# Performance work log

Measured on AMD Instinct MI355X. Metric: run time of the kernel, lower is better.

The kernel has to match this reference:

```python
import jax, jax.numpy as jnp
import numpy as np

EPS = 1e-5  # torch LayerNorm default

def ln(x, g, b):
    mu = jnp.mean(x, axis=-1, keepdims=True)
    var = jnp.mean((x - mu) ** 2, axis=-1, keepdims=True)
    return (x - mu) * jax.lax.rsqrt(var + EPS) * g + b

B, S, E, A = 131072, 199, 3, 32
D_IN = S + 1  # state_dim + 1 (time feature)

def setup_inputs() -> dict:
    key = jax.random.key(0)
    ks = iter(jax.random.split(key, 32))
    def w(shape, fan_in):
        lim = 1.0 / np.sqrt(fan_in)
        return jax.random.uniform(next(ks), shape, jnp.float32, -lim, lim)
    inp = {
        "state": jax.random.normal(next(ks), (B, S), jnp.float32),
        "time_delta": jax.random.uniform(next(ks), (B,), jnp.float32),
        # trunk: Linear(200,256)+LN, Linear(256,256)+LN, Linear(256,128)+LN
        "W1": w((D_IN, 256), D_IN), "b1": w((256,), D_IN),
        "g1": jnp.ones((256,), jnp.float32), "be1": jnp.zeros((256,), jnp.float32),
        "W2": w((256, 256), 256), "b2": w((256,), 256),
        "g2": jnp.ones((256,), jnp.float32), "be2": jnp.zeros((256,), jnp.float32),
        "W3": w((256, 128), 256), "b3": w((128,), 256),
        "g3": jnp.ones((128,), jnp.float32), "be3": jnp.zeros((128,), jnp.float32),
        # value stream
        "Wv1": w((128, 64), 128), "bv1": w((64,), 128),
        "gv": jnp.ones((64,), jnp.float32), "bev": jnp.zeros((64,), jnp.float32),
        "Wv2": w((64, 1), 64), "bv2": w((1,), 64),
        # E stacked advantage streams (all heads share action dim A)
        "Wa1": w((E, 128, 64), 128), "ba1": w((E, 64), 128),
        "ga": jnp.ones((E, 64), jnp.float32), "bea": jnp.zeros((E, 64), jnp.float32),
        "Wa2": w((E, 64, A), 64), "ba2": w((E, A), 64),
        "event_type": jax.random.randint(next(ks), (B,), 0, E),
    }
    return inp

def reference(state, time_delta,
              W1, b1, g1, be1, W2, b2, g2, be2, W3, b3, g3, be3,
              Wv1, bv1, gv, bev, Wv2, bv2,
              Wa1, ba1, ga, bea, Wa2, ba2, event_type):
    td = time_delta[:, None]                       # [B,1]
    x = jnp.concatenate([state, td], axis=1)       # [B,200]
    h = jax.nn.relu(ln(x @ W1 + b1, g1, be1))      # [B,256]
    h = jax.nn.relu(ln(h @ W2 + b2, g2, be2))      # [B,256]
    f = jax.nn.relu(ln(h @ W3 + b3, g3, be3))      # [B,128]
    v = jax.nn.relu(ln(f @ Wv1 + bv1, gv, bev)) @ Wv2 + bv2  # [B,1]
    # compute all E advantage heads, then per-sample select by event_type
    h1 = jnp.einsum('bd,edh->ebh', f, Wa1) + ba1[:, None, :]           # [E,B,64]
    h1 = jax.nn.relu(ln(h1, ga[:, None, :], bea[:, None, :]))
    adv_all = jnp.einsum('ebh,eha->eba', h1, Wa2) + ba2[:, None, :]    # [E,B,A]
    adv = jnp.take_along_axis(adv_all, event_type[None, :, None], axis=0)[0]  # [B,A]
    return v + (adv - adv.mean(axis=1, keepdims=True))
```

## Files before the change

kernel.cpp:

```cpp
#include <hip/hip_runtime.h>
#include <stdint.h>

#define DEV __device__ __forceinline__

typedef __attribute__((ext_vector_type(8))) short short8;
typedef __attribute__((ext_vector_type(4))) short short4v;
typedef __attribute__((ext_vector_type(4))) float floatx4;

constexpr int TM  = 64;
constexpr int NB  = 131072;
constexpr int AST = 264;

constexpr int OFF_W1 = 0;
constexpr int OFF_W2 = 57344;
constexpr int OFF_W3 = 122880;
constexpr int OFF_WH = 155648;
constexpr int OFF_WA2= 188416;
constexpr int NWQ    = 194560;

constexpr int C_B1=0, C_G1=256, C_BE1=512, C_B2=768, C_G2=1024, C_BE2=1280,
  C_B3=1536, C_G3=1664, C_BE3=1792, C_BV1=1920, C_GV=1984, C_BEV=2048,
  C_WV2=2112, C_BV2=2176, C_BA1=2177, C_GA=2369, C_BEA=2561, C_BA2=2753;
constexpr int NCONST=2849;

struct Ptrs {
  const float *state,*td,*W1,*b1,*g1,*be1,*W2,*b2,*g2,*be2,*W3,*b3,*g3,*be3,
    *Wv1,*bv1,*gv,*bev,*Wv2,*bv2,*Wa1,*ba1,*ga,*bea,*Wa2,*ba2;
  const int *et;
};

DEV unsigned short f2bf(float x){
  uint32_t u = __float_as_uint(x);
  u += 0x7fffu + ((u>>16)&1u);
  return (unsigned short)(u>>16);
}

__global__ void prep_kernel(Ptrs p, unsigned short* __restrict__ wq, float* __restrict__ cq){
  int idx = blockIdx.x*256 + threadIdx.x;
  if (idx < NWQ) {
    float v = 0.f;
    if (idx < OFF_W2) {
      int e = idx, w = e/14336, r = e%14336;
      int kc = r>>11, ct=(r>>9)&3, l=(r>>3)&63, j=r&7;
      int n = w*64 + ct*16 + (l&15);
      int k = kc*32 + (l>>4)*8 + j;
      if (k < 200) v = p.W1[k*256 + n];
    } else if (idx < OFF_W3) {
      int e = idx-OFF_W2, w=e>>14, r=e&16383;
      int kc=r>>11, ct=(r>>9)&3, l=(r>>3)&63, j=r&7;
      int n = w*64 + ct*16 + (l&15);
      int k = kc*32 + (l>>4)*8 + j;
      int c = (k & ~63) + 16*(k&3) + ((k&63)>>2);
      v = p.W2[c*256 + n];
    } else if (idx < OFF_WH) {
      int e = idx-OFF_W3, w=e>>13, r=e&8191;
      int kc=r>>10, ct=(r>>9)&1, l=(r>>3)&63, j=r&7;
      int n = w*32 + ct*16 + (l&15);
      int k = kc*32 + (l>>4)*8 + j;
      int c = (k & ~63) + 16*(k&3) + ((k&63)>>2);
      v = p.W3[c*128 + n];
    } else if (idx < OFF_WA2) {
      int e = idx-OFF_WH, h=e>>13, r=e&8191;
      int kc=r>>11, ct=(r>>9)&3, l=(r>>3)&63, j=r&7;
      int n = ct*16 + (l&15);
      int k = kc*32 + (l>>4)*8 + j;
      int c = (k & ~31) + 16*(k&1) + ((k&31)>>1);
      v = (h<3) ? p.Wa1[h*8192 + c*64 + n] : p.Wv1[c*64 + n];
    } else {
      int e = idx-OFF_WA2, h=e>>11, r=e&2047;
      int kc=r>>10, ct=(r>>9)&1, l=(r>>3)&63, j=r&7;
      int n = ct*16 + (l&15);
      int k = kc*32 + (l>>4)*8 + j;
      int c = 16*(k&3) + (k>>2);
      v = p.Wa2[h*2048 + c*32 + n];
    }
    wq[idx] = f2bf(v);
  } else if (idx < NWQ + NCONST) {
    int ci = idx - NWQ;
    const float* src; int off;
    if      (ci < 256)  { src=p.b1;  off=ci; }
    else if (ci < 512)  { src=p.g1;  off=ci-256; }
    else if (ci < 768)  { src=p.be1; off=ci-512; }
    else if (ci < 1024) { src=p.b2;  off=ci-768; }
    else if (ci < 1280) { src=p.g2;  off=ci-1024; }
    else if (ci < 1536) { src=p.be2; off=ci-1280; }
    else if (ci < 1664) { src=p.b3;  off=ci-1536; }
    else if (ci < 1792) { src=p.g3;  off=ci-1664; }
    else if (ci < 1920) { src=p.be3; off=ci-1792; }
    else if (ci < 1984) { src=p.bv1; off=ci-1920; }
    else if (ci < 2048) { src=p.gv;  off=ci-1984; }
    else if (ci < 2112) { src=p.bev; off=ci-2048; }
    else if (ci < 2176) { src=p.Wv2; off=ci-2112; }
    else if (ci < 2177) { src=p.bv2; off=ci-2176; }
    else if (ci < 2369) { src=p.ba1; off=ci-2177; }
    else if (ci < 2561) { src=p.ga;  off=ci-2369; }
    else if (ci < 2753) { src=p.bea; off=ci-2561; }
    else                { src=p.ba2; off=ci-2753; }
    cq[ci] = src[off];
  }
}

template<int N>
DEV void loadB(short8 (&B)[N], const unsigned short* __restrict__ src, int lane){
  #pragma unroll
  for (int i=0;i<N;i++) B[i] = *(const short8*)(src + i*512 + lane*8);
}

template<int RT,int CT>
DEV void zeroAcc(floatx4 (&acc)[RT][CT]){
  const floatx4 z = {0.f,0.f,0.f,0.f};
  #pragma unroll
  for (int rt=0;rt<RT;rt++)
    #pragma unroll
    for (int ct=0;ct<CT;ct++) acc[rt][ct]=z;
}

template<int KC,int CT>
DEV void runGemm(floatx4 (&acc)[4][CT], const short8 (&B)[KC*CT],
                 const unsigned short* aBase, int aOff){
  #pragma unroll
  for (int kc=0;kc<KC;kc++){
    short8 a[4];
    #pragma unroll
    for (int rt=0;rt<4;rt++)
      a[rt] = *(const short8*)(aBase + rt*16*AST + aOff + kc*32);
    #pragma unroll
    for (int rt=0;rt<4;rt++)
      #pragma unroll
      for (int ct=0;ct<CT;ct++)
        acc[rt][ct] = __builtin_amdgcn_mfma_f32_16x16x32_bf16(a[rt], B[kc*CT+ct], acc[rt][ct], 0,0,0);
  }
}

template<int CT>
DEV void biasStatsWrite(floatx4 (&acc)[4][CT], const float* __restrict__ cq, int bo, int colBase,
                        float2* pstatw, int ln, int q){
  float bias[CT];
  #pragma unroll
  for (int ct=0;ct<CT;ct++) bias[ct]=cq[bo+colBase+ct*16+ln];
  #pragma unroll
  for (int rt=0;rt<4;rt++){
    float s[4]={0,0,0,0}, ss[4]={0,0,0,0};
    #pragma unroll
    for (int ct=0;ct<CT;ct++){
      #pragma unroll
      for (int r=0;r<4;r++){
        float v=acc[rt][ct][r]+bias[ct];
        acc[rt][ct][r]=v; s[r]+=v; ss[r]+=v*v;
      }
    }
    #pragma unroll
    for (int r=0;r<4;r++){
      #pragma unroll
      for (int d=1;d<16;d<<=1){ s[r]+=__shfl_xor(s[r],d); ss[r]+=__shfl_xor(ss[r],d); }
      if (ln==0) pstatw[rt*16+q*4+r] = make_float2(s[r], ss[r]);
    }
  }
}

template<int CT>
DEV void lnWrite(floatx4 (&acc)[4][CT], const float* __restrict__ cq, int go, int beo, int colBase,
                 const float2* fstat, unsigned short* act_, int ln, int q){
  float g[CT], be[CT];
  #pragma unroll
  for (int ct=0;ct<CT;ct++){ g[ct]=cq[go+colBase+ct*16+ln]; be[ct]=cq[beo+colBase+ct*16+ln]; }
  #pragma unroll
  for (int rt=0;rt<4;rt++){
    #pragma unroll
    for (int r=0;r<4;r++){
      int row=rt*16+q*4+r;
      float2 st=fstat[row];
      unsigned short* pp = act_ + row*AST + colBase + ln*CT;
      if constexpr (CT==4){
        short4v vv;
        #pragma unroll
        for (int ct=0;ct<CT;ct++){
          float y=(acc[rt][ct][r]-st.x)*st.y*g[ct]+be[ct];
          vv[ct]=(short)f2bf(fmaxf(y,0.f));
        }
        *(short4v*)pp = vv;
      } else {
        uint32_t pk=0;
        #pragma unroll
        for (int ct=0;ct<CT;ct++){
          float y=(acc[rt][ct][r]-st.x)*st.y*g[ct]+be[ct];
          pk |= ((uint32_t)f2bf(fmaxf(y,0.f)))<<(16*ct);
        }
        *(uint32_t*)pp = pk;
      }
    }
  }
}

__global__ __launch_bounds__(256,2) void dqn_main(
    const float* __restrict__ state, const float* __restrict__ td,
    const int* __restrict__ et, const unsigned short* __restrict__ wq,
    const float* __restrict__ cq, float* __restrict__ out)
{
  __shared__ __align__(16) unsigned short act[TM*AST];
  __shared__ float2 pstat[4*64];
  __shared__ float2 fstat[64];
  __shared__ float  advbuf[64*32];
  __shared__ float  vbuf[64];
  __shared__ int    etl[64];

  const int tid=threadIdx.x, w=tid>>6, lane=tid&63, q=lane>>4, ln=lane&15;
  const int rowBlk = blockIdx.x*TM;

  {
    int r = tid>>2, q4 = tid&3, c0 = q4*56;
    const float* srow = state + (size_t)(rowBlk+r)*199;
    float tdv = td[rowBlk+r];
    unsigned short* arow = act + r*AST;
    #pragma unroll
    for (int cc=0; cc<28; cc++){
      int c = c0 + cc*2;
      float v0 = (c  <199)? srow[c]   : (c  ==199? tdv : 0.f);
      float v1 = (c+1<199)? srow[c+1] : (c+1==199? tdv : 0.f);
      uint32_t pk = (uint32_t)f2bf(v0) | ((uint32_t)f2bf(v1)<<16);
      *(uint32_t*)(arow + c) = pk;
    }
    if (tid < 64) etl[tid] = et[rowBlk+tid];
  }
  __syncthreads();

  const unsigned short* aBase = act + ln*AST + q*8;
  floatx4 acc[4][4];

  {
    short8 B[28];
    loadB<28>(B, wq + OFF_W1 + w*14336, lane);
    zeroAcc<4,4>(acc);
    runGemm<7,4>(acc, B, aBase, 0);
  }
  biasStatsWrite<4>(acc, cq, C_B1, w*64, &pstat[w*64], ln, q);
  __syncthreads();
  if (tid<64){
    float s=0, ss=0;
    #pragma unroll
    for (int ww=0;ww<4;ww++){ float2 pp=pstat[ww*64+tid]; s+=pp.x; ss+=pp.y; }
    float mu=s*(1.f/256.f), var=ss*(1.f/256.f)-mu*mu;
    fstat[tid]=make_float2(mu, rsqrtf(var+1e-5f));
  }
  __syncthreads();
  lnWrite<4>(acc, cq, C_G1, C_BE1, w*64, fstat, act, ln, q);
  __syncthreads();

  {
    short8 B[32];
    loadB<32>(B, wq + OFF_W2 + w*16384, lane);
    zeroAcc<4,4>(acc);
    runGemm<8,4>(acc, B, aBase, 0);
  }
  biasStatsWrite<4>(acc, cq, C_B2, w*64, &pstat[w*64], ln, q);
  __syncthreads();
  if (tid<64){
    float s=0, ss=0;
    #pragma unroll
    for (int ww=0;ww<4;ww++){ float2 pp=pstat[ww*64+tid]; s+=pp.x; ss+=pp.y; }
    float mu=s*(1.f/256.f), var=ss*(1.f/256.f)-mu*mu;
    fstat[tid]=make_float2(mu, rsqrtf(var+1e-5f));
  }
  __syncthreads();
  lnWrite<4>(acc, cq, C_G2, C_BE2, w*64, fstat, act, ln, q);
  __syncthreads();

  {
    floatx4 acc2[4][2];
    {
      short8 B[16];
      loadB<16>(B, wq + OFF_W3 + w*8192, lane);
      zeroAcc<4,2>(acc2);
      runGemm<8,2>(acc2, B, aBase, 0);
    }
    biasStatsWrite<2>(acc2, cq, C_B3, w*32, &pstat[w*64], ln, q);
    __syncthreads();
    if (tid<64){
      float s=0, ss=0;
      #pragma unroll
      for (int ww=0;ww<4;ww++){ float2 pp=pstat[ww*64+tid]; s+=pp.x; ss+=pp.y; }
      float mu=s*(1.f/128.f), var=ss*(1.f/128.f)-mu*mu;
      fstat[tid]=make_float2(mu, rsqrtf(var+1e-5f));
    }
    __syncthreads();
    lnWrite<2>(acc2, cq, C_G3, C_BE3, w*32, fstat, act, ln, q);
    __syncthreads();
  }

  {
    short8 B[16];
    loadB<16>(B, wq + OFF_WH + w*8192, lane);
    zeroAcc<4,4>(acc);
    runGemm<4,4>(acc, B, aBase, 0);
  }
  {
    const int bo = (w<3)? C_BA1+w*64 : C_BV1;
    const int go = (w<3)? C_GA +w*64 : C_GV;
    const int beo= (w<3)? C_BEA+w*64 : C_BEV;
    float bias[4], g[4], be[4];
    #pragma unroll
    for (int ct=0;ct<4;ct++){ bias[ct]=cq[bo+ct*16+ln]; g[ct]=cq[go+ct*16+ln]; be[ct]=cq[beo+ct*16+ln]; }
    #pragma unroll
    for (int rt=0;rt<4;rt++){
      float s[4]={0,0,0,0}, ss[4]={0,0,0,0};
      #pragma unroll
      for (int ct=0;ct<4;ct++)
        #pragma unroll
        for (int r=0;r<4;r++){
          float v=acc[rt][ct][r]+bias[ct];
          acc[rt][ct][r]=v; s[r]+=v; ss[r]+=v*v;
        }
      float mu[4], rs[4];
      #pragma unroll
      for (int r=0;r<4;r++){
        #pragma unroll
        for (int d=1;d<16;d<<=1){ s[r]+=__shfl_xor(s[r],d); ss[r]+=__shfl_xor(ss[r],d); }
        mu[r]=s[r]*(1.f/64.f);
        rs[r]=rsqrtf(ss[r]*(1.f/64.f)-mu[r]*mu[r]+1e-5f);
      }
      #pragma unroll
      for (int ct=0;ct<4;ct++)
        #pragma unroll
        for (int r=0;r<4;r++)
          acc[rt][ct][r]=fmaxf((acc[rt][ct][r]-mu[r])*rs[r]*g[ct]+be[ct], 0.f);
    }
  }

  if (w==3){
    float wv[4];
    #pragma unroll
    for (int ct=0;ct<4;ct++) wv[ct]=cq[C_WV2+ct*16+ln];
    float bv2v = cq[C_BV2];
    #pragma unroll
    for (int rt=0;rt<4;rt++){
      float dd[4]={0,0,0,0};
      #pragma unroll
      for (int ct=0;ct<4;ct++)
        #pragma unroll
        for (int r=0;r<4;r++) dd[r]+=acc[rt][ct][r]*wv[ct];
      #pragma unroll
      for (int r=0;r<4;r++){
        #pragma unroll
        for (int d=1;d<16;d<<=1) dd[r]+=__shfl_xor(dd[r],d);
        if (ln==0) vbuf[rt*16+q*4+r]=dd[r]+bv2v;
      }
    }
  }
  __syncthreads();

  if (w<3){
    #pragma unroll
    for (int rt=0;rt<4;rt++)
      #pragma unroll
      for (int r=0;r<4;r++){
        int row=rt*16+q*4+r;
        unsigned short* pp = act + row*AST + 64*w + ln*4;
        short4v vv;
        #pragma unroll
        for (int ct=0;ct<4;ct++) vv[ct]=(short)f2bf(acc[rt][ct][r]);
        *(short4v*)pp = vv;
      }
    short8 B2[4];
    loadB<4>(B2, wq + OFF_WA2 + w*2048, lane);
    floatx4 a2[4][2];
    zeroAcc<4,2>(a2);
    runGemm<2,2>(a2, B2, aBase, 64*w);
    #pragma unroll
    for (int ct=0;ct<2;ct++){
      float b2v = cq[C_BA2 + w*32 + ct*16 + ln];
      #pragma unroll
      for (int rt=0;rt<4;rt++)
        #pragma unroll
        for (int r=0;r<4;r++){
          int row=rt*16+q*4+r;
          if (etl[row]==w) advbuf[row*32 + ct*16 + ln] = a2[rt][ct][r] + b2v;
        }
    }
  }
  __syncthreads();

  if (tid<64){
    float s=0;
    #pragma unroll
    for (int cc=0;cc<32;cc++){ int c=(cc+tid)&31; s+=advbuf[tid*32+c]; }
    fstat[tid].x = s*(1.f/32.f);
  }
  __syncthreads();
  {
    int row = tid>>2, c0=(tid&3)*8;
    float v = vbuf[row], m = fstat[row].x;
    float4 o0, o1;
    o0.x = v + advbuf[row*32+c0+0] - m;  o0.y = v + advbuf[row*32+c0+1] - m;
    o0.z = v + advbuf[row*32+c0+2] - m;  o0.w = v + advbuf[row*32+c0+3] - m;
    o1.x = v + advbuf[row*32+c0+4] - m;  o1.y = v + advbuf[row*32+c0+5] - m;
    o1.z = v + advbuf[row*32+c0+6] - m;  o1.w = v + advbuf[row*32+c0+7] - m;
    float* op = out + (size_t)(rowBlk+row)*32 + c0;
    *(float4*)op = o0;
    *(float4*)(op+4) = o1;
  }
}

extern "C" void kernel_launch(void* const* d_in, const int* in_sizes, int n_in,
                              void* d_out, int out_size, void* d_ws, size_t ws_size,
                              hipStream_t stream)
{
  Ptrs p;
  p.state=(const float*)d_in[0];  p.td =(const float*)d_in[1];
  p.W1 =(const float*)d_in[2];  p.b1 =(const float*)d_in[3];  p.g1 =(const float*)d_in[4];  p.be1=(const float*)d_in[5];
  p.W2 =(const float*)d_in[6];  p.b2 =(const float*)d_in[7];  p.g2 =(const float*)d_in[8];  p.be2=(const float*)d_in[9];
  p.W3 =(const float*)d_in[10]; p.b3 =(const float*)d_in[11]; p.g3 =(const float*)d_in[12]; p.be3=(const float*)d_in[13];
  p.Wv1=(const float*)d_in[14]; p.bv1=(const float*)d_in[15]; p.gv =(const float*)d_in[16]; p.bev=(const float*)d_in[17];
  p.Wv2=(const float*)d_in[18]; p.bv2=(const float*)d_in[19];
  p.Wa1=(const float*)d_in[20]; p.ba1=(const float*)d_in[21]; p.ga =(const float*)d_in[22]; p.bea=(const float*)d_in[23];
  p.Wa2=(const float*)d_in[24]; p.ba2=(const float*)d_in[25];
  p.et =(const int*)d_in[26];

  unsigned short* wq = (unsigned short*)d_ws;
  float* cq = (float*)((char*)d_ws + (size_t)NWQ*2);

  const int prepN = NWQ + NCONST;
  hipLaunchKernelGGL(prep_kernel, dim3((prepN+255)/256), dim3(256), 0, stream, p, wq, cq);
  hipLaunchKernelGGL(dqn_main, dim3(NB/TM), dim3(256), 0, stream,
                     p.state, p.td, p.et, (const unsigned short*)wq, (const float*)cq, (float*)d_out);
}
```

Measured before the change: 341.5 us.

## Raise occupancy to 3 blocks/CU, reuse accumulator array, coalesce state staging

Raises launch bounds from 2 to 3 blocks per CU. To fit the tighter register budget it reuses the single 4x4 accumulator array for the narrower layer-3 and advantage GEMMs. Float-to-bf16 conversion now uses the packed hardware intrinsic for two values at once. The input staging loop is rewritten so consecutive threads read consecutive floats of the state block instead of each thread walking its own row. The higher occupancy could force register spills, since the 28-32 B fragments are held in registers, and the staging loop adds integer division.

```diff
diff --git a/kernel.cpp b/kernel.cpp
--- a/kernel.cpp
+++ b/kernel.cpp
@@ -1,10 +1,10 @@
 #include <hip/hip_runtime.h>
+#include <hip/hip_bf16.h>
 #include <stdint.h>
 
 #define DEV __device__ __forceinline__
 
 typedef __attribute__((ext_vector_type(8))) short short8;
-typedef __attribute__((ext_vector_type(4))) short short4v;
 typedef __attribute__((ext_vector_type(4))) float floatx4;
 
 constexpr int TM  = 64;
@@ -33,6 +33,12 @@
   uint32_t u = __float_as_uint(x);
   u += 0x7fffu + ((u>>16)&1u);
   return (unsigned short)(u>>16);
+}
+DEV uint32_t f2bf_pk(float a, float b){
+  float2 f2; f2.x=a; f2.y=b;
+  __hip_bfloat162 h = __float22bfloat162_rn(f2);
+  union { __hip_bfloat162 h; uint32_t u; } cv; cv.h = h;
+  return cv.u;
 }
 
 __global__ void prep_kernel(Ptrs p, unsigned short* __restrict__ wq, float* __restrict__ cq){
@@ -106,17 +112,17 @@
   for (int i=0;i<N;i++) B[i] = *(const short8*)(src + i*512 + lane*8);
 }
 
-template<int RT,int CT>
-DEV void zeroAcc(floatx4 (&acc)[RT][CT]){
+template<int CT>
+DEV void zeroAcc(floatx4 (&acc)[4][4]){
   const floatx4 z = {0.f,0.f,0.f,0.f};
   #pragma unroll
-  for (int rt=0;rt<RT;rt++)
+  for (int rt=0;rt<4;rt++)
     #pragma unroll
     for (int ct=0;ct<CT;ct++) acc[rt][ct]=z;
 }
 
 template<int KC,int CT>
-DEV void runGemm(floatx4 (&acc)[4][CT], const short8 (&B)[KC*CT],
+DEV void runGemm(floatx4 (&acc)[4][4], const short8 (&B)[KC*CT],
                  const unsigned short* aBase, int aOff){
   #pragma unroll
   for (int kc=0;kc<KC;kc++){
@@ -133,7 +139,7 @@
 }
 
 template<int CT>
-DEV void biasStatsWrite(floatx4 (&acc)[4][CT], const float* __restrict__ cq, int bo, int colBase,
+DEV void biasStatsWrite(floatx4 (&acc)[4][4], const float* __restrict__ cq, int bo, int colBase,
                         float2* pstatw, int ln, int q){
   float bias[CT];
   #pragma unroll
@@ -159,7 +165,7 @@
 }
 
 template<int CT>
-DEV void lnWrite(floatx4 (&acc)[4][CT], const float* __restrict__ cq, int go, int beo, int colBase,
+DEV void lnWrite(floatx4 (&acc)[4][4], const float* __restrict__ cq, int go, int beo, int colBase,
                  const float2* fstat, unsigned short* act_, int ln, int q){
   float g[CT], be[CT];
   #pragma unroll
@@ -171,28 +177,21 @@
       int row=rt*16+q*4+r;
       float2 st=fstat[row];
       unsigned short* pp = act_ + row*AST + colBase + ln*CT;
+      float y[CT];
+      #pragma unroll
+      for (int ct=0;ct<CT;ct++)
+        y[ct] = fmaxf((acc[rt][ct][r]-st.x)*st.y*g[ct]+be[ct], 0.f);
       if constexpr (CT==4){
-        short4v vv;
-        #pragma unroll
-        for (int ct=0;ct<CT;ct++){
-          float y=(acc[rt][ct][r]-st.x)*st.y*g[ct]+be[ct];
-          vv[ct]=(short)f2bf(fmaxf(y,0.f));
-        }
-        *(short4v*)pp = vv;
+        uint2 pk; pk.x = f2bf_pk(y[0],y[1]); pk.y = f2bf_pk(y[2],y[3]);
+        *(uint2*)pp = pk;
       } else {
-        uint32_t pk=0;
-        #pragma unroll
-        for (int ct=0;ct<CT;ct++){
-          float y=(acc[rt][ct][r]-st.x)*st.y*g[ct]+be[ct];
-          pk |= ((uint32_t)f2bf(fmaxf(y,0.f)))<<(16*ct);
-        }
-        *(uint32_t*)pp = pk;
+        *(uint32_t*)pp = f2bf_pk(y[0],y[1]);
       }
     }
   }
 }
 
-__global__ __launch_bounds__(256,2) void dqn_main(
+__global__ __launch_bounds__(256,3) void dqn_main(
     const float* __restrict__ state, const float* __restrict__ td,
     const int* __restrict__ et, const unsigned short* __restrict__ wq,
     const float* __restrict__ cq, float* __restrict__ out)
@@ -208,17 +207,17 @@
   const int rowBlk = blockIdx.x*TM;
 
   {
-    int r = tid>>2, q4 = tid&3, c0 = q4*56;
-    const float* srow = state + (size_t)(rowBlk+r)*199;
-    float tdv = td[rowBlk+r];
-    unsigned short* arow = act + r*AST;
-    #pragma unroll
-    for (int cc=0; cc<28; cc++){
-      int c = c0 + cc*2;
-      float v0 = (c  <199)? srow[c]   : (c  ==199? tdv : 0.f);
-      float v1 = (c+1<199)? srow[c+1] : (c+1==199? tdv : 0.f);
-      uint32_t pk = (uint32_t)f2bf(v0) | ((uint32_t)f2bf(v1)<<16);
-      *(uint32_t*)(arow + c) = pk;
+    const float* sbase = state + (size_t)rowBlk*199;
+    for (int i=tid; i<64*199; i+=256){
+      float v = sbase[i];
+      int row = i/199, col = i - row*199;
+      act[row*AST+col] = f2bf(v);
+    }
+    for (int i=tid; i<64*25; i+=256){
+      int row = i/25, c = 199 + (i - row*25);
+      unsigned short hv = 0;
+      if (c==199) hv = f2bf(td[rowBlk+row]);
+      act[row*AST+c] = hv;
     }
     if (tid < 64) etl[tid] = et[rowBlk+tid];
   }
@@ -230,7 +229,7 @@
   {
     short8 B[28];
     loadB<28>(B, wq + OFF_W1 + w*14336, lane);
-    zeroAcc<4,4>(acc);
+    zeroAcc<4>(acc);
     runGemm<7,4>(acc, B, aBase, 0);
   }
   biasStatsWrite<4>(acc, cq, C_B1, w*64, &pstat[w*64], ln, q);
@@ -249,7 +248,7 @@
   {
     short8 B[32];
     loadB<32>(B, wq + OFF_W2 + w*16384, lane);
-    zeroAcc<4,4>(acc);
+    zeroAcc<4>(acc);
     runGemm<8,4>(acc, B, aBase, 0);
   }
   biasStatsWrite<4>(acc, cq, C_B2, w*64, &pstat[w*64], ln, q);
@@ -266,31 +265,28 @@
   __syncthreads();
 
   {
-    floatx4 acc2[4][2];
-    {
-      short8 B[16];
-      loadB<16>(B, wq + OFF_W3 + w*8192, lane);
-      zeroAcc<4,2>(acc2);
-      runGemm<8,2>(acc2, B, aBase, 0);
-    }
-    biasStatsWrite<2>(acc2, cq, C_B3, w*32, &pstat[w*64], ln, q);
-    __syncthreads();
-    if (tid<64){
-      float s=0, ss=0;
-      #pragma unroll
-      for (int ww=0;ww<4;ww++){ float2 pp=pstat[ww*64+tid]; s+=pp.x; ss+=pp.y; }
-      float mu=s*(1.f/128.f), var=ss*(1.f/128.f)-mu*mu;
-      fstat[tid]=make_float2(mu, rsqrtf(var+1e-5f));
-    }
-    __syncthreads();
-    lnWrite<2>(acc2, cq, C_G3, C_BE3, w*32, fstat, act, ln, q);
-    __syncthreads();
-  }
+    short8 B[16];
+    loadB<16>(B, wq + OFF_W3 + w*8192, lane);
+    zeroAcc<2>(acc);
+    runGemm<8,2>(acc, B, aBase, 0);
+  }
+  biasStatsWrite<2>(acc, cq, C_B3, w*32, &pstat[w*64], ln, q);
+  __syncthreads();
+  if (tid<64){
+    float s=0, ss=0;
+    #pragma unroll
+    for (int ww=0;ww<4;ww++){ float2 pp=pstat[ww*64+tid]; s+=pp.x; ss+=pp.y; }
+    float mu=s*(1.f/128.f), var=ss*(1.f/128.f)-mu*mu;
+    fstat[tid]=make_float2(mu, rsqrtf(var+1e-5f));
+  }
+  __syncthreads();
+  lnWrite<2>(acc, cq, C_G3, C_BE3, w*32, fstat, act, ln, q);
+  __syncthreads();
 
   {
     short8 B[16];
     loadB<16>(B, wq + OFF_WH + w*8192, lane);
-    zeroAcc<4,4>(acc);
+    zeroAcc<4>(acc);
     runGemm<4,4>(acc, B, aBase, 0);
   }
   {
@@ -355,16 +351,15 @@
       for (int r=0;r<4;r++){
         int row=rt*16+q*4+r;
         unsigned short* pp = act + row*AST + 64*w + ln*4;
-        short4v vv;
-        #pragma unroll
-        for (int ct=0;ct<4;ct++) vv[ct]=(short)f2bf(acc[rt][ct][r]);
-        *(short4v*)pp = vv;
+        uint2 pk;
+        pk.x = f2bf_pk(acc[rt][0][r], acc[rt][1][r]);
+        pk.y = f2bf_pk(acc[rt][2][r], acc[rt][3][r]);
+        *(uint2*)pp = pk;
       }
     short8 B2[4];
     loadB<4>(B2, wq + OFF_WA2 + w*2048, lane);
-    floatx4 a2[4][2];
-    zeroAcc<4,2>(a2);
-    runGemm<2,2>(a2, B2, aBase, 64*w);
+    zeroAcc<2>(acc);
+    runGemm<2,2>(acc, B2, aBase, 64*w);
     #pragma unroll
     for (int ct=0;ct<2;ct++){
       float b2v = cq[C_BA2 + w*32 + ct*16 + ln];
@@ -373,7 +368,7 @@
         #pragma unroll
         for (int r=0;r<4;r++){
           int row=rt*16+q*4+r;
-          if (etl[row]==w) advbuf[row*32 + ct*16 + ln] = a2[rt][ct][r] + b2v;
+          if (etl[row]==w) advbuf[row*32 + ct*16 + ln] = acc[rt][ct][r] + b2v;
         }
     }
   }
```

Measured after the change: 320.3 us. -6.2%, faster.
